# Kernel optimization log

Measured on AMD Instinct MI355X. Metric: run time of the kernel, lower is better.

The kernel has to match this reference:

```python
import jax, jax.numpy as jnp
from jax import lax
import numpy as np

STRIDE = 1
PADDING = 1
DILATION = 1


def setup_inputs() -> dict:
    key = jax.random.key(0)
    k1, k2, k3, k4 = jax.random.split(key, 4)
    B, Cin, Cout, H, W, K, G = 32, 256, 256, 56, 56, 3, 8
    x = jax.random.normal(k1, (B, Cin, H, W), dtype=jnp.float32)
    conv = jax.random.normal(k2, (Cout, Cin, K, K), dtype=jnp.float32)
    S = jax.random.normal(k3, (Cin, G), dtype=jnp.float32)
    T = jax.random.normal(k4, (Cout, G), dtype=jnp.float32)
    return {"x": x, "conv": conv, "S": S, "T": T}


def reference(x, conv, S, T):
    # Faithful to FLGC.forward (training path).
    Cin = S.shape[0]
    Cout = T.shape[0]
    s_hat = jax.nn.softmax(S, axis=1)            # [Cin, G]
    t_hat = jax.nn.softmax(T, axis=1)            # [Cout, G]
    s = jnp.argmax(s_hat, axis=1)                # group id per input channel
    t = jnp.argmax(t_hat, axis=1)                # group id per output filter
    # Input channel c is scaled by s_hat[c, s[c]] inside its group.
    x_sc = x * s_hat[jnp.arange(Cin), s][None, :, None, None]
    # Filter o uses weight conv[o,c] * t_hat[o, t[o]] only where s[c] == t[o];
    # masking weights to zero elsewhere makes one dense conv equal the per-group convs.
    gate = (s[None, :] == t[:, None]).astype(conv.dtype)          # [Cout, Cin]
    w = conv * t_hat[jnp.arange(Cout), t][:, None, None, None] * gate[:, :, None, None]
    out_full = lax.conv_general_dilated(
        x_sc, w,
        window_strides=(STRIDE, STRIDE),
        padding=[(PADDING, PADDING), (PADDING, PADDING)],
        rhs_dilation=(DILATION, DILATION),
    )  # [B, Cout, H', W'], channel o = group-conv output of filter o
    # Original concatenates group outputs (channels ordered by perm = stable sort of t),
    # then indexes that with perm again: final[:, j] = out_full[:, perm[perm[j]]].
    perm = jnp.argsort(t * Cout + jnp.arange(Cout))  # stable group-major order
    return out_full[:, perm[perm]]
```

## Files before the change

### kernel.cpp

```cpp
#include <hip/hip_runtime.h>

#define M_SI    0
#define M_SO    256
#define M_CLIST 512
#define M_FLIST 768
#define M_DEST  1024
#define M_CBASE 1280
#define M_FBASE 1288
#define M_CCNT  1296
#define M_FCNT  1304
#define M_WOFFE 1312
#define WPACK_BYTE_OFF 16384
#define XR_BYTE_OFF   (4u << 20)
#define SLOT_ELEMS    3444736ull
#define SLOT_BYTES    (SLOT_ELEMS * 2ull)

typedef short bf16x8 __attribute__((ext_vector_type(8)));
typedef float f32x4  __attribute__((ext_vector_type(4)));

__device__ __forceinline__ unsigned short f2bf(float f) {
    unsigned u = __float_as_uint(f);
    u += 0x7fffu + ((u >> 16) & 1u);
    return (unsigned short)(u >> 16);
}

__device__ __forceinline__ void gl_lds16(const void* g, void* l) {
    __builtin_amdgcn_global_load_lds((const __attribute__((address_space(1))) unsigned int*)g,
                                     (__attribute__((address_space(3))) unsigned int*)l, 16, 0, 0);
}

__global__ __launch_bounds__(256) void flgc_setup(const float* __restrict__ S,
                                                  const float* __restrict__ T,
                                                  int* __restrict__ meta) {
    __shared__ float si[256], so[256];
    __shared__ int gin[256], gout[256];
    __shared__ int cnt_in[8], cnt_out[8], cb[8], fb[8];
    __shared__ int perm[256], destl[256];
    const int c = threadIdx.x;

    {
        float m = S[c * 8]; int am = 0;
        for (int k = 1; k < 8; ++k) { float v = S[c * 8 + k]; if (v > m) { m = v; am = k; } }
        float s = 0.f;
        for (int k = 0; k < 8; ++k) s += expf(S[c * 8 + k] - m);
        si[c] = 1.0f / s; gin[c] = am;
    }
    {
        float m = T[c * 8]; int am = 0;
        for (int k = 1; k < 8; ++k) { float v = T[c * 8 + k]; if (v > m) { m = v; am = k; } }
        float s = 0.f;
        for (int k = 0; k < 8; ++k) s += expf(T[c * 8 + k] - m);
        so[c] = 1.0f / s; gout[c] = am;
    }
    __syncthreads();
    const int g = gin[c], go = gout[c];
    int r1 = 0, r2 = 0;
    for (int i = 0; i < c; ++i) { r1 += (gin[i] == g); r2 += (gout[i] == go); }
    if (c < 8) {
        int n1 = 0, n2 = 0;
        for (int i = 0; i < 256; ++i) { n1 += (gin[i] == c); n2 += (gout[i] == c); }
        cnt_in[c] = n1; cnt_out[c] = n2;
    }
    __syncthreads();
    if (c == 0) {
        int a = 0, b = 0;
        for (int k = 0; k < 8; ++k) { cb[k] = a; a += cnt_in[k]; fb[k] = b; b += cnt_out[k]; }
    }
    __syncthreads();
    meta[M_CLIST + cb[g] + r1] = c;
    perm[fb[go] + r2] = c;
    __syncthreads();
    const int ppc = perm[perm[c]];
    destl[ppc] = c;
    __syncthreads();
    ((float*)meta)[M_SI + c] = si[c];
    ((float*)meta)[M_SO + c] = so[c];
    meta[M_FLIST + c] = perm[c];
    meta[M_DEST + c]  = destl[c];
    if (c < 8) {
        meta[M_CBASE + c] = cb[c];
        meta[M_FBASE + c] = fb[c];
        meta[M_CCNT + c]  = cnt_in[c];
        meta[M_FCNT + c]  = cnt_out[c];
    }
    if (c == 0) {
        int a = 0;
        for (int k = 0; k < 8; ++k) {
            meta[M_WOFFE + k] = a;
            const int nq  = (cnt_in[k] + 31) >> 5;
            const int mfa = (cnt_out[k] + 15) >> 4;
            a += nq * mfa * 9 * 512;
        }
        meta[M_WOFFE + 8] = a;
    }
}

__global__ void flgc_pack(const float* __restrict__ conv, const int* __restrict__ meta,
                          unsigned short* __restrict__ wpack) {
    const float* si = (const float*)meta + M_SI;
    const float* so = (const float*)meta + M_SO;
    const int total = meta[M_WOFFE + 8];
    for (int idx = blockIdx.x * blockDim.x + threadIdx.x; idx < total;
         idx += gridDim.x * blockDim.x) {
        int gg = 0;
        while (gg < 7 && idx >= meta[M_WOFFE + gg + 1]) ++gg;
        const int local = idx - meta[M_WOFFE + gg];
        const int fcnt = meta[M_FCNT + gg], ccnt = meta[M_CCNT + gg];
        const int mfall = (fcnt + 15) >> 4;
        const int fragidx = local >> 9, e = local & 511;
        const int lane = e >> 3, j = e & 7;
        const int tap = fragidx % 9, t2 = fragidx / 9;
        const int mf = t2 % mfall, q = t2 / mfall;
        const int fl = mf * 16 + (lane & 15);
        const int cl = q * 32 + (lane >> 4) * 8 + j;
        float v = 0.f;
        if (fl < fcnt && cl < ccnt) {
            const int F  = meta[M_FLIST + meta[M_FBASE + gg] + fl];
            const int CH = meta[M_CLIST + meta[M_CBASE + gg] + cl];
            v = conv[(F * 256 + CH) * 9 + tap] * si[CH] * so[F];
        }
        wpack[idx] = f2bf(v);
    }
}

__global__ __launch_bounds__(256) void flgc_reorder(const float* __restrict__ x,
                                                    const int* __restrict__ meta,
                                                    unsigned short* __restrict__ xr) {
    __shared__ __align__(16) float lds[8448];
    const int bx = blockIdx.x;
    const int b = blockIdx.y;
    const int slot = blockIdx.z;
    const int g = slot >> 1, q = slot & 1;
    const int ccnt = meta[M_CCNT + g];
    int nq = (ccnt + 31) >> 5; if (nq > 2) nq = 2;
    if (q >= nq) return;
    const int cbas = meta[M_CBASE + g];
    const int tid = threadIdx.x, lane = tid & 63, wv = tid >> 6;

    {
        const int xrow0 = 4 * bx + wv - 1;
        const int xrow = (xrow0 < 0) ? 0 : ((xrow0 > 55) ? 55 : xrow0);
        const int i = lane >> 4;
        int col4 = (lane & 15) * 4; if (col4 > 52) col4 = 52;
        const float* xb = x + (size_t)b * 802816 + (size_t)xrow * 56 + col4;
        for (int j = 0; j < 8; ++j) {
            const int cgl = q * 32 + 4 * j + i;
            const int ch = meta[M_CLIST + cbas + ((cgl < ccnt) ? cgl : 0)];
            gl_lds16(xb + (size_t)ch * 3136, (char*)lds + (wv * 8 + j) * 1056);
        }
    }
    __syncthreads();

    unsigned short* dstb = xr + (size_t)(slot * 32 + b) * 107648ull;
    if (tid < 32) {
        const int rr = tid >> 3, rem = tid & 7;
        const int r = 4 * bx + rr;
        if (r < 58) {
            const int col = (rem >> 2) ? 57 : 0;
            const int sl = rem & 3;
            *(ushort4*)&dstb[(size_t)r * 1856 + col * 32 + sl * 4] = make_ushort4(0, 0, 0, 0);
        }
    }
    for (int k = tid; k < 448; k += 256) {
        const int rr = k / 112, rem = k - rr * 112;
        const int chq = rem / 14, aq = rem - chq * 14;
        const int r = 4 * bx + rr;
        if (r >= 58) continue;
        const int xrow0 = r - 1;
        const bool rowok = (unsigned)xrow0 < 56u;
        f32x4 vv[4];
#pragma unroll
        for (int i = 0; i < 4; ++i) {
            vv[i] = *(const f32x4*)&lds[(rr * 8 + chq) * 264 + i * 64 + 4 * aq];
            const int cgl = q * 32 + 4 * chq + i;
            if (!rowok || cgl >= ccnt) vv[i] = (f32x4){0.f, 0.f, 0.f, 0.f};
        }
        const int c16 = chq >> 1, lo = (chq & 1) * 4;
        unsigned short* dr = dstb + (size_t)r * 1856;
#pragma unroll
        for (int kk = 0; kk < 4; ++kk) {
            const int col = 4 * aq + 1 + kk;
            const int s16 = c16 ^ ((col >> 1) & 3);
            ushort4 pk = make_ushort4(f2bf(vv[0][kk]), f2bf(vv[1][kk]),
                                      f2bf(vv[2][kk]), f2bf(vv[3][kk]));
            *(ushort4*)&dr[col * 32 + s16 * 8 + lo] = pk;
        }
    }
}

template <int MFE>
__device__ __forceinline__ void conv_pass(
    const unsigned short* __restrict__ wpack, const unsigned short* __restrict__ xr,
    float* __restrict__ out, unsigned short* xbufA, unsigned short* xbufB,
    const int (&ocv)[3][4], int b, int g, int z, int nq, int mf0, int mfall, int woffe,
    int lane, int wv) {
    const int nn = lane & 15, kg = lane >> 4;
    int addrc[4][3];
#pragma unroll
    for (int cg = 0; cg < 4; ++cg)
#pragma unroll
        for (int dc = 0; dc < 3; ++dc) {
            int ccol = cg * 16 + nn + dc; if (ccol > 57) ccol = 57;
            addrc[cg][dc] = (ccol << 6) + ((kg ^ ((ccol >> 1) & 3)) << 4);
        }
    const int ns = (z < 2) ? 4 : 3;
    const int P = ns * nq;
    const int base = wv * 348;
    {
        const char* src = (const char*)(xr + (size_t)((g * 2) * 32 + b) * 107648ull
                                        + (size_t)(4 * z) * 1856);
        char* dstb = (char*)xbufA;
#pragma unroll
        for (int j = 0; j < 5; ++j)
            gl_lds16(src + (size_t)(base + j * 64 + lane) * 16, dstb + (base + j * 64) * 16);
        if (lane < 28)
            gl_lds16(src + (size_t)(base + 320 + lane) * 16, dstb + (base + 320) * 16);
    }
    f32x4 acc[MFE][4];
    for (int p = 0; p < P; ++p) {
        const int q = (nq == 2) ? (p & 1) : 0;
        const int s = z + 4 * ((nq == 2) ? (p >> 1) : p);
        bf16x8 A[MFE][9];
        {
            const unsigned short* ap =
                wpack + woffe + ((size_t)(q * mfall + mf0) * 9) * 512 + lane * 8;
#pragma unroll
            for (int mf = 0; mf < MFE; ++mf)
#pragma unroll
                for (int tap = 0; tap < 9; ++tap)
                    A[mf][tap] = *(const bf16x8*)(ap + (size_t)(mf * 9 + tap) * 512);
        }
        __builtin_amdgcn_sched_barrier(0);
        if (p + 1 < P) {
            const int pn = p + 1;
            const int qp = (nq == 2) ? (pn & 1) : 0;
            const int sp = z + 4 * ((nq == 2) ? (pn >> 1) : pn);
            const char* src = (const char*)(xr + (size_t)((g * 2 + qp) * 32 + b) * 107648ull
                                            + (size_t)(4 * sp) * 1856);
            char* dstb = (char*)((pn & 1) ? xbufB : xbufA);
#pragma unroll
            for (int j = 0; j < 5; ++j)
                gl_lds16(src + (size_t)(base + j * 64 + lane) * 16, dstb + (base + j * 64) * 16);
            if (lane < 28)
                gl_lds16(src + (size_t)(base + 320 + lane) * 16, dstb + (base + 320) * 16);
            asm volatile("s_waitcnt vmcnt(6)" ::: "memory");
        } else {
            asm volatile("s_waitcnt vmcnt(0)" ::: "memory");
        }
        __builtin_amdgcn_s_barrier();
        __builtin_amdgcn_sched_barrier(0);
        const unsigned short* xb = (p & 1) ? xbufB : xbufA;
        if (q == 0) {
#pragma unroll
            for (int mf = 0; mf < MFE; ++mf)
#pragma unroll
                for (int cg = 0; cg < 4; ++cg) acc[mf][cg] = (f32x4){0.f, 0.f, 0.f, 0.f};
        }
#pragma unroll
        for (int tap = 0; tap < 9; ++tap) {
            const int dr = tap / 3, dc = tap - dr * 3;
            const int rowb = ((wv + dr) * 58) << 6;
#pragma unroll
            for (int cg = 0; cg < 4; ++cg) {
                const bf16x8 Bv = *(const bf16x8*)((const char*)xb + rowb + addrc[cg][dc]);
#pragma unroll
                for (int mf = 0; mf < MFE; ++mf)
                    acc[mf][cg] = __builtin_amdgcn_mfma_f32_16x16x32_bf16(
                        A[mf][tap], Bv, acc[mf][cg], 0, 0, 0);
            }
        }
        if (q == nq - 1) {
            const int h = 4 * s + wv;
#pragma unroll
            for (int mf = 0; mf < MFE; ++mf)
#pragma unroll
                for (int reg = 0; reg < 4; ++reg) {
                    const int oc = ocv[mf][reg];
                    if (oc >= 0) {
                        float* op = out + ((size_t)(b * 256 + oc) * 56 + h) * 56;
#pragma unroll
                        for (int cg = 0; cg < 4; ++cg) {
                            const int col = cg * 16 + nn;
                            if (col < 56) op[col] = acc[mf][cg][reg];
                        }
                    }
                }
        }
        __builtin_amdgcn_sched_barrier(0);
        __builtin_amdgcn_s_barrier();
    }
}

__global__ __launch_bounds__(256, 2) void flgc_conv_r(const int* __restrict__ meta,
                                                      const unsigned short* __restrict__ wpack,
                                                      const unsigned short* __restrict__ xr,
                                                      float* __restrict__ out) {
    __shared__ __align__(16) unsigned short xbufA[11136];
    __shared__ __align__(16) unsigned short xbufB[11136];
    const int b = blockIdx.x, g = blockIdx.y, z = blockIdx.z;
    const int tid = threadIdx.x, lane = tid & 63, wv = tid >> 6;
    const int ccnt = meta[M_CCNT + g], fcnt = meta[M_FCNT + g];
    const int fbas = meta[M_FBASE + g], woffe = meta[M_WOFFE + g];
    int nq = (ccnt + 31) >> 5; if (nq > 2) nq = 2;
    const int mfall = (fcnt + 15) >> 4;
    if (mfall == 0) return;
    const int nn = lane & 15;

    for (int mf0 = 0; mf0 < mfall; mf0 += 3) {
        const int mfe = min(3, mfall - mf0);
        int ocv[3][4];
#pragma unroll
        for (int mf = 0; mf < 3; ++mf)
#pragma unroll
            for (int reg = 0; reg < 4; ++reg) {
                const int fl = (mf0 + mf) * 16 + (lane >> 4) * 4 + reg;
                ocv[mf][reg] = (mf < mfe && fl < fcnt)
                    ? meta[M_DEST + meta[M_FLIST + fbas + fl]] : -1;
            }
        if (nq == 0) {
            const int ns = (z < 2) ? 4 : 3;
            for (int si = 0; si < ns; ++si) {
                const int h = 4 * (z + 4 * si) + wv;
#pragma unroll
                for (int mf = 0; mf < 3; ++mf)
#pragma unroll
                    for (int reg = 0; reg < 4; ++reg)
                        if (ocv[mf][reg] >= 0) {
                            float* op = out + ((size_t)(b * 256 + ocv[mf][reg]) * 56 + h) * 56;
#pragma unroll
                            for (int cg = 0; cg < 4; ++cg) {
                                const int col = cg * 16 + nn;
                                if (col < 56) op[col] = 0.f;
                            }
                        }
            }
            continue;
        }
        if (mfe == 3)      conv_pass<3>(wpack, xr, out, xbufA, xbufB, ocv, b, g, z, nq, mf0, mfall, woffe, lane, wv);
        else if (mfe == 2) conv_pass<2>(wpack, xr, out, xbufA, xbufB, ocv, b, g, z, nq, mf0, mfall, woffe, lane, wv);
        else               conv_pass<1>(wpack, xr, out, xbufA, xbufB, ocv, b, g, z, nq, mf0, mfall, woffe, lane, wv);
    }
}

__global__ __launch_bounds__(256, 2) void flgc_conv_mfma(const float* __restrict__ x,
                                                         const int* __restrict__ meta,
                                                         const unsigned short* __restrict__ wpack,
                                                         float* __restrict__ out) {
    __shared__ __align__(16) unsigned short xlds[10 * 4 * 64 * 8];
    __shared__ __align__(16) unsigned short wlds[4 * 9 * 512];
    const int g = blockIdx.z, b = blockIdx.y, h0 = blockIdx.x * 8;
    const int tid = threadIdx.x, lane = tid & 63, wv = tid >> 6;
    const int ccnt = meta[M_CCNT + g], fcnt = meta[M_FCNT + g];
    const int cbas = meta[M_CBASE + g], fbas = meta[M_FBASE + g];
    const int woffe = meta[M_WOFFE + g];
    const int nq = (ccnt + 31) >> 5, mfall = (fcnt + 15) >> 4;
    if (mfall == 0) return;
    const int n = lane & 15, kgl = lane >> 4;
    const int prow = 2 * wv + (n >> 3);
    const int pcol = n & 7;

    for (int mf0 = 0; mf0 < mfall; mf0 += 4) {
        const int mfe = min(4, mfall - mf0);
        f32x4 acc[4][7];
#pragma unroll
        for (int mf = 0; mf < 4; ++mf)
#pragma unroll
            for (int cg = 0; cg < 7; ++cg) acc[mf][cg] = (f32x4){0.f, 0.f, 0.f, 0.f};

        for (int q = 0; q < nq; ++q) {
            __syncthreads();
            for (int widx = wv; widx < mfe * 9; widx += 4) {
                const int mf = widx / 9, tap = widx - mf * 9;
                const unsigned short* src =
                    wpack + woffe + (((q * mfall) + mf0 + mf) * 9 + tap) * 512 + lane * 8;
                *(bf16x8*)&wlds[(mf * 9 + tap) * 512 + lane * 8] = *(const bf16x8*)src;
            }
            for (int i = tid; i < 80 * 64; i += 256) {
                const int colx = i & 63, t = i >> 6;
                const int rr = t >> 3, cq = t & 7;
                const int c0 = q * 32 + cq * 4;
                const int row = h0 + rr - 1, ic = colx - 1;
                float v0 = 0.f, v1 = 0.f, v2 = 0.f, v3 = 0.f;
                if ((unsigned)row < 56u && (unsigned)ic < 56u) {
                    const float* xp = x + (size_t)(b * 256) * 3136 + row * 56 + ic;
                    if (c0 + 0 < ccnt) v0 = xp[(size_t)meta[M_CLIST + cbas + c0 + 0] * 3136];
                    if (c0 + 1 < ccnt) v1 = xp[(size_t)meta[M_CLIST + cbas + c0 + 1] * 3136];
                    if (c0 + 2 < ccnt) v2 = xp[(size_t)meta[M_CLIST + cbas + c0 + 2] * 3136];
                    if (c0 + 3 < ccnt) v3 = xp[(size_t)meta[M_CLIST + cbas + c0 + 3] * 3136];
                }
                ushort4 pk = make_ushort4(f2bf(v0), f2bf(v1), f2bf(v2), f2bf(v3));
                *(ushort4*)&xlds[(((rr * 4 + (cq >> 1)) * 64 + colx) << 3) + ((cq & 1) << 2)] = pk;
            }
            __syncthreads();
#pragma unroll
            for (int tap = 0; tap < 9; ++tap) {
                const int dr = tap / 3, dcp = tap - dr * 3;
                bf16x8 A[4];
#pragma unroll
                for (int mf = 0; mf < 4; ++mf)
                    if (mf < mfe)
                        A[mf] = *(bf16x8*)&wlds[(mf * 9 + tap) * 512 + lane * 8];
                const int row_r = prow + dr;
                const int xbase = ((row_r * 4 + kgl) * 64) << 3;
#pragma unroll
                for (int cg = 0; cg < 7; ++cg) {
                    const int cc = cg * 8 + pcol + dcp;
                    const bf16x8 B = *(bf16x8*)&xlds[xbase + (cc << 3)];
#pragma unroll
                    for (int mf = 0; mf < 4; ++mf)
                        if (mf < mfe)
                            acc[mf][cg] = __builtin_amdgcn_mfma_f32_16x16x32_bf16(
                                A[mf], B, acc[mf][cg], 0, 0, 0);
                }
            }
        }
#pragma unroll
        for (int mf = 0; mf < 4; ++mf) {
            if (mf < mfe) {
#pragma unroll
                for (int reg = 0; reg < 4; ++reg) {
                    const int fl = (mf0 + mf) * 16 + (lane >> 4) * 4 + reg;
                    if (fl < fcnt) {
                        const int F  = meta[M_FLIST + fbas + fl];
                        const int oc = meta[M_DEST + F];
                        float* op = out + ((size_t)(b * 256 + oc) * 56 + (h0 + prow)) * 56 + pcol;
#pragma unroll
                        for (int cg = 0; cg < 7; ++cg)
                            op[cg * 8] = acc[mf][cg][reg];
                    }
                }
            }
        }
    }
}

extern "C" void kernel_launch(void* const* d_in, const int* in_sizes, int n_in,
                              void* d_out, int out_size, void* d_ws, size_t ws_size,
                              hipStream_t stream) {
    const float* x    = (const float*)d_in[0];
    const float* conv = (const float*)d_in[1];
    const float* S    = (const float*)d_in[2];
    const float* T    = (const float*)d_in[3];
    float* out = (float*)d_out;
    int* meta = (int*)d_ws;
    unsigned short* wpack = (unsigned short*)((char*)d_ws + WPACK_BYTE_OFF);
    unsigned short* xr    = (unsigned short*)((char*)d_ws + XR_BYTE_OFF);

    flgc_setup<<<1, 256, 0, stream>>>(S, T, meta);
    flgc_pack<<<256, 256, 0, stream>>>(conv, meta, wpack);

    const size_t need = (size_t)XR_BYTE_OFF + 16ull * SLOT_BYTES + 65536;
    if (ws_size >= need) {
        flgc_reorder<<<dim3(15, 32, 16), 256, 0, stream>>>(x, meta, xr);
        flgc_conv_r<<<dim3(32, 8, 4), 256, 0, stream>>>(meta, wpack, xr, out);
    } else {
        flgc_conv_mfma<<<dim3(7, 32, 8), 256, 0, stream>>>(x, meta, wpack, out);
    }
}
```

Measured before the change: 111.6 us.

## Pipeline reorder kernel with double-buffered LDS over row pairs per block

```diff
diff --git a/kernel.cpp b/kernel.cpp
--- a/kernel.cpp
+++ b/kernel.cpp
@@ -123,69 +123,89 @@
     }
 }
 
-__global__ __launch_bounds__(256) void flgc_reorder(const float* __restrict__ x,
-                                                    const int* __restrict__ meta,
-                                                    unsigned short* __restrict__ xr) {
-    __shared__ __align__(16) float lds[8448];
-    const int bx = blockIdx.x;
-    const int b = blockIdx.y;
-    const int slot = blockIdx.z;
+__global__ __launch_bounds__(256, 4) void flgc_reorder(const float* __restrict__ x,
+                                                       const int* __restrict__ meta,
+                                                       unsigned short* __restrict__ xr) {
+    __shared__ __align__(16) float lds[2][4224];
+    const int b = blockIdx.x;
+    const int slot = blockIdx.y;
+    const int half = blockIdx.z;
     const int g = slot >> 1, q = slot & 1;
     const int ccnt = meta[M_CCNT + g];
     int nq = (ccnt + 31) >> 5; if (nq > 2) nq = 2;
     if (q >= nq) return;
     const int cbas = meta[M_CBASE + g];
     const int tid = threadIdx.x, lane = tid & 63, wv = tid >> 6;
-
-    {
-        const int xrow0 = 4 * bx + wv - 1;
-        const int xrow = (xrow0 < 0) ? 0 : ((xrow0 > 55) ? 55 : xrow0);
-        const int i = lane >> 4;
-        int col4 = (lane & 15) * 4; if (col4 > 52) col4 = 52;
-        const float* xb = x + (size_t)b * 802816 + (size_t)xrow * 56 + col4;
-        for (int j = 0; j < 8; ++j) {
-            const int cgl = q * 32 + 4 * j + i;
-            const int ch = meta[M_CLIST + cbas + ((cgl < ccnt) ? cgl : 0)];
-            gl_lds16(xb + (size_t)ch * 3136, (char*)lds + (wv * 8 + j) * 1056);
-        }
-    }
-    __syncthreads();
-
+    const int t0 = half ? 15 : 0, t1 = half ? 29 : 15;
+    const float* xb0 = x + (size_t)b * 802816;
     unsigned short* dstb = xr + (size_t)(slot * 32 + b) * 107648ull;
-    if (tid < 32) {
-        const int rr = tid >> 3, rem = tid & 7;
-        const int r = 4 * bx + rr;
-        if (r < 58) {
-            const int col = (rem >> 2) ? 57 : 0;
-            const int sl = rem & 3;
-            *(ushort4*)&dstb[(size_t)r * 1856 + col * 32 + sl * 4] = make_ushort4(0, 0, 0, 0);
-        }
-    }
-    for (int k = tid; k < 448; k += 256) {
-        const int rr = k / 112, rem = k - rr * 112;
-        const int chq = rem / 14, aq = rem - chq * 14;
-        const int r = 4 * bx + rr;
-        if (r >= 58) continue;
-        const int xrow0 = r - 1;
-        const bool rowok = (unsigned)xrow0 < 56u;
-        f32x4 vv[4];
-#pragma unroll
-        for (int i = 0; i < 4; ++i) {
-            vv[i] = *(const f32x4*)&lds[(rr * 8 + chq) * 264 + i * 64 + 4 * aq];
-            const int cgl = q * 32 + 4 * chq + i;
-            if (!rowok || cgl >= ccnt) vv[i] = (f32x4){0.f, 0.f, 0.f, 0.f};
-        }
-        const int c16 = chq >> 1, lo = (chq & 1) * 4;
-        unsigned short* dr = dstb + (size_t)r * 1856;
-#pragma unroll
-        for (int kk = 0; kk < 4; ++kk) {
-            const int col = 4 * aq + 1 + kk;
-            const int s16 = c16 ^ ((col >> 1) & 3);
-            ushort4 pk = make_ushort4(f2bf(vv[0][kk]), f2bf(vv[1][kk]),
-                                      f2bf(vv[2][kk]), f2bf(vv[3][kk]));
-            *(ushort4*)&dr[col * 32 + s16 * 8 + lo] = pk;
-        }
-    }
+
+    const int si_ = lane >> 4;
+    int col4 = (lane & 15) * 4; if (col4 > 52) col4 = 52;
+    int chnl[8];
+#pragma unroll
+    for (int chg = 0; chg < 8; ++chg) {
+        const int cgl = q * 32 + 4 * chg + si_;
+        chnl[chg] = meta[M_CLIST + cbas + ((cgl < ccnt) ? cgl : 0)];
+    }
+
+#define STAGE(T, BF)                                                                     \
+    {                                                                                    \
+        _Pragma("unroll") for (int j = 0; j < 4; ++j) {                                  \
+            const int seg = wv * 4 + j;                                                  \
+            const int rr = seg >> 3, chg = seg & 7;                                      \
+            const int xrow0 = 2 * (T) + rr - 1;                                          \
+            const int xrow = (xrow0 < 0) ? 0 : ((xrow0 > 55) ? 55 : xrow0);              \
+            gl_lds16(xb0 + (size_t)chnl[chg] * 3136 + xrow * 56 + col4,                  \
+                     (char*)&lds[BF][0] + seg * 1056);                                   \
+        }                                                                                \
+    }
+
+    STAGE(t0, 0);
+    for (int t = t0; t < t1; ++t) {
+        const int cur = (t - t0) & 1;
+        if (t + 1 < t1) {
+            STAGE(t + 1, cur ^ 1);
+            asm volatile("s_waitcnt vmcnt(4)" ::: "memory");
+        } else {
+            asm volatile("s_waitcnt vmcnt(0)" ::: "memory");
+        }
+        __builtin_amdgcn_s_barrier();
+        __builtin_amdgcn_sched_barrier(0);
+        if (tid < 32) {
+            const int rr = tid >> 4, rem = tid & 15;
+            const int col = (rem >> 3) ? 57 : 0;
+            const int sl = rem & 7;
+            *(ushort4*)&dstb[(size_t)(2 * t + rr) * 1856 + col * 32 + sl * 4] =
+                make_ushort4(0, 0, 0, 0);
+        }
+        if (tid < 224) {
+            const int rr = tid / 112, rem = tid - rr * 112;
+            const int chq = rem / 14, aq = rem - chq * 14;
+            const int r = 2 * t + rr;
+            const bool rowok = (unsigned)(r - 1) < 56u;
+            f32x4 vv[4];
+#pragma unroll
+            for (int i = 0; i < 4; ++i) {
+                vv[i] = *(const f32x4*)&lds[cur][(rr * 8 + chq) * 264 + i * 64 + 4 * aq];
+                const int cgl = q * 32 + 4 * chq + i;
+                if (!rowok || cgl >= ccnt) vv[i] = (f32x4){0.f, 0.f, 0.f, 0.f};
+            }
+            const int c16 = chq >> 1, lo = (chq & 1) * 4;
+            unsigned short* dr = dstb + (size_t)r * 1856;
+#pragma unroll
+            for (int kk = 0; kk < 4; ++kk) {
+                const int col = 4 * aq + 1 + kk;
+                const int s16 = c16 ^ ((col >> 1) & 3);
+                ushort4 pk = make_ushort4(f2bf(vv[0][kk]), f2bf(vv[1][kk]),
+                                          f2bf(vv[2][kk]), f2bf(vv[3][kk]));
+                *(ushort4*)&dr[col * 32 + s16 * 8 + lo] = pk;
+            }
+        }
+        __builtin_amdgcn_sched_barrier(0);
+        __builtin_amdgcn_s_barrier();
+    }
+#undef STAGE
 }
 
 template <int MFE>
@@ -451,7 +471,7 @@
 
     const size_t need = (size_t)XR_BYTE_OFF + 16ull * SLOT_BYTES + 65536;
     if (ws_size >= need) {
-        flgc_reorder<<<dim3(15, 32, 16), 256, 0, stream>>>(x, meta, xr);
+        flgc_reorder<<<dim3(32, 16, 2), 256, 0, stream>>>(x, meta, xr);
         flgc_conv_r<<<dim3(32, 8, 4), 256, 0, stream>>>(meta, wpack, xr, out);
     } else {
         flgc_conv_mfma<<<dim3(7, 32, 8), 256, 0, stream>>>(x, meta, wpack, out);
```

New measurement: 131.4 us. 17.8% more time.
